# Performance work log

Measured on AMD Instinct MI355X. Metric: run time of the kernel, lower is better.

Reference implementation:

```python
import jax, jax.numpy as jnp
import numpy as np

NUM_SEGMENTS = 4480  # BATCH_SIZE * MAX_ATOMS = 64 * 70
ATOM_DIM = 64
BOND_DIM = 16
N_EDGES = 65536


def setup_inputs() -> dict:
    key = jax.random.key(0)
    k1, k2, k3, k4 = jax.random.split(key, 4)
    atom_feat = jax.random.normal(k1, (NUM_SEGMENTS, ATOM_DIM), dtype=jnp.float32)
    bond_feat = jax.random.normal(k2, (N_EDGES, BOND_DIM), dtype=jnp.float32)
    pair_idx = jax.random.randint(k3, (N_EDGES, 2), 0, NUM_SEGMENTS, dtype=jnp.int64)
    # glorot-uniform style kernel, zero bias (as in add_weight initializers)
    limit = float(np.sqrt(6.0 / (BOND_DIM + ATOM_DIM ** 2)))
    kernel = jax.random.uniform(k4, (BOND_DIM, ATOM_DIM ** 2), dtype=jnp.float32,
                                minval=-limit, maxval=limit)
    bias = jnp.zeros((ATOM_DIM ** 2,), dtype=jnp.float32)
    return {"atom_feat": atom_feat, "bond_feat": bond_feat,
            "pair_idx": pair_idx, "kernel": kernel, "bias": bias}


def reference(atom_feat, bond_feat, pair_idx, kernel, bias):
    atom_dim = atom_feat.shape[-1]
    # dense projection of bond features -> per-edge transform matrices
    bond_transformed = bond_feat @ kernel + bias               # [E, D*D]
    bond_transformed = bond_transformed.reshape(-1, atom_dim, atom_dim)  # [E, D, D]
    # gather neighbor (source) atom features per edge
    neighbor_feat = jnp.take(atom_feat, pair_idx[:, 1].astype(jnp.int32), axis=0)  # [E, D]
    # per-edge matrix-vector product
    messages = jnp.einsum('eij,ej->ei', bond_transformed, neighbor_feat)  # [E, D]
    # scatter-add into destination atoms
    return jax.ops.segment_sum(messages, pair_idx[:, 0].astype(jnp.int32),
                               num_segments=NUM_SEGMENTS)  # [NUM_SEGMENTS, D]
```

## Files before the change

kernel.cpp:

```cpp
#include <hip/hip_runtime.h>

#define NSEG   4480
#define ADIM   64
#define BDIM   16
#define NEDGE  65536
#define DPB    16
#define NBLK   (NSEG / DPB)
#define TPB    1024
#define CAP    64
#define GSP    1096

#define CNT_OFF  (4u << 20)

typedef __bf16 bf16x8 __attribute__((ext_vector_type(8)));
typedef float  f32x4  __attribute__((ext_vector_type(4)));

__device__ __forceinline__ unsigned short f2bf(float f) {
    union { float f; unsigned int i; } c; c.f = f;
    unsigned int x = c.i;
    x += 0x7fffu + ((x >> 16) & 1u);
    return (unsigned short)(x >> 16);
}

union U8 { unsigned short u[8]; bf16x8 v; };

__device__ __forceinline__ bf16x8 pack_bf8(float4 a, float4 b) {
    U8 r;
    r.u[0] = f2bf(a.x); r.u[1] = f2bf(a.y); r.u[2] = f2bf(a.z); r.u[3] = f2bf(a.w);
    r.u[4] = f2bf(b.x); r.u[5] = f2bf(b.y); r.u[6] = f2bf(b.z); r.u[7] = f2bf(b.w);
    return r.v;
}

__global__ __launch_bounds__(256) void scatter_kernel(
    const int* __restrict__ pair, int* __restrict__ cnt, int2* __restrict__ eb)
{
    const int e  = blockIdx.x * 256 + threadIdx.x;
    const int2 p = ((const int2*)pair)[e];
    const int idx = atomicAdd(&cnt[p.x], 1);
    if (idx < CAP) eb[(size_t)p.x * CAP + idx] = make_int2(e, p.y);
}

__global__ __launch_bounds__(TPB) void fused_kernel(
    const float* __restrict__ atom,
    const float* __restrict__ bond,
    const int*   __restrict__ cnt,
    const int2*  __restrict__ eb,
    const float* __restrict__ kern,
    const float* __restrict__ bias,
    float*       __restrict__ out)
{
    __shared__ unsigned short Gs[DPB * GSP];

    const int t    = threadIdx.x;
    const int lane = t & 63;
    const int w    = t >> 6;
    const int dlo  = blockIdx.x * DPB;
    const int d    = dlo + w;

    {
        int n = cnt[d];
        n = n < CAP ? n : CAP;
        const int2 my = eb[(size_t)d * CAP + lane];

        float g[17];
#pragma unroll
        for (int r = 0; r < 17; ++r) g[r] = 0.f;

        int k = 0;
        for (; k + 2 <= n; k += 2) {
            const int e0 = __builtin_amdgcn_readlane(my.x, k);
            const int s0 = __builtin_amdgcn_readlane(my.y, k);
            const int e1 = __builtin_amdgcn_readlane(my.x, k + 1);
            const int s1 = __builtin_amdgcn_readlane(my.y, k + 1);
            const float a0 = atom[(size_t)s0 * ADIM + lane];
            const float a1 = atom[(size_t)s1 * ADIM + lane];
            const float4* b0p = (const float4*)(bond + (size_t)e0 * BDIM);
            const float4* b1p = (const float4*)(bond + (size_t)e1 * BDIM);
            const float4 c0 = b0p[0], c1 = b0p[1], c2 = b0p[2], c3 = b0p[3];
            const float4 d0 = b1p[0], d1 = b1p[1], d2 = b1p[2], d3 = b1p[3];
            const float bb0[16] = { c0.x,c0.y,c0.z,c0.w, c1.x,c1.y,c1.z,c1.w,
                                    c2.x,c2.y,c2.z,c2.w, c3.x,c3.y,c3.z,c3.w };
            const float bb1[16] = { d0.x,d0.y,d0.z,d0.w, d1.x,d1.y,d1.z,d1.w,
                                    d2.x,d2.y,d2.z,d2.w, d3.x,d3.y,d3.z,d3.w };
#pragma unroll
            for (int r = 0; r < 16; ++r) g[r] = fmaf(a0, bb0[r], g[r]);
            g[16] += a0;
#pragma unroll
            for (int r = 0; r < 16; ++r) g[r] = fmaf(a1, bb1[r], g[r]);
            g[16] += a1;
        }
        if (k < n) {
            const int e0 = __builtin_amdgcn_readlane(my.x, k);
            const int s0 = __builtin_amdgcn_readlane(my.y, k);
            const float a0 = atom[(size_t)s0 * ADIM + lane];
            const float4* b0p = (const float4*)(bond + (size_t)e0 * BDIM);
            const float4 c0 = b0p[0], c1 = b0p[1], c2 = b0p[2], c3 = b0p[3];
            const float bb0[16] = { c0.x,c0.y,c0.z,c0.w, c1.x,c1.y,c1.z,c1.w,
                                    c2.x,c2.y,c2.z,c2.w, c3.x,c3.y,c3.z,c3.w };
#pragma unroll
            for (int r = 0; r < 16; ++r) g[r] = fmaf(a0, bb0[r], g[r]);
            g[16] += a0;
        }

#pragma unroll
        for (int r = 0; r < 17; ++r)
            Gs[w * GSP + r * 64 + lane] = f2bf(g[r]);
    }
    __syncthreads();

    if (w < 4) {
        const int m    = lane & 15;
        const int quad = lane >> 4;
        const int c    = w * 16 + m;
        const unsigned short* Ga = Gs + (size_t)m * GSP;

        f32x4 acc = {0.f, 0.f, 0.f, 0.f};

        const float* ks0 = kern + (size_t)c * 64 + quad * 8;
        float4 x0 = *(const float4*)(ks0);
        float4 x1 = *(const float4*)(ks0 + 4);
        float4 y0 = *(const float4*)(ks0 + 32);
        float4 y1 = *(const float4*)(ks0 + 36);

#pragma unroll
        for (int r = 0; r < 17; ++r) {
            float4 nx0, nx1, ny0, ny1;
            if (r + 1 < 17) {
                const float* ns = ((r + 1 < 16) ? (kern + (size_t)(r + 1) * 4096)
                                                : bias)
                                  + (size_t)c * 64 + quad * 8;
                nx0 = *(const float4*)(ns);
                nx1 = *(const float4*)(ns + 4);
                ny0 = *(const float4*)(ns + 32);
                ny1 = *(const float4*)(ns + 36);
            }
            const bf16x8 a0 = *(const bf16x8*)(Ga + r * 64 + quad * 8);
            const bf16x8 a1 = *(const bf16x8*)(Ga + r * 64 + 32 + quad * 8);
            acc = __builtin_amdgcn_mfma_f32_16x16x32_bf16(a0, pack_bf8(x0, x1), acc, 0, 0, 0);
            acc = __builtin_amdgcn_mfma_f32_16x16x32_bf16(a1, pack_bf8(y0, y1), acc, 0, 0, 0);
            x0 = nx0; x1 = nx1; y0 = ny0; y1 = ny1;
        }

#pragma unroll
        for (int rr = 0; rr < 4; ++rr)
            out[(size_t)(dlo + quad * 4 + rr) * ADIM + c] = acc[rr];
    }
}

extern "C" void kernel_launch(void* const* d_in, const int* in_sizes, int n_in,
                              void* d_out, int out_size, void* d_ws, size_t ws_size,
                              hipStream_t stream) {
    const float* atom = (const float*)d_in[0];
    const float* bond = (const float*)d_in[1];
    const int*   pair = (const int*)  d_in[2];
    const float* kern = (const float*)d_in[3];
    const float* bias = (const float*)d_in[4];
    float* out = (float*)d_out;

    int2* eb = (int2*)d_ws;
    int*  cnt = (int*)((char*)d_ws + CNT_OFF);

    hipMemsetAsync(cnt, 0, NSEG * sizeof(int), stream);
    scatter_kernel<<<NEDGE / 256, 256, 0, stream>>>(pair, cnt, eb);
    fused_kernel<<<NBLK, TPB, 0, stream>>>(atom, bond, cnt, eb, kern, bias, out);
}
```

Baseline: 92.19 us.

## Fuse memset, scatter and compute into one cooperative kernel with grid syncs

Result: slower. 240.4 us (+160.8%).

```diff
diff --git a/kernel.cpp b/kernel.cpp
--- a/kernel.cpp
+++ b/kernel.cpp
@@ -1,10 +1,13 @@
 #include <hip/hip_runtime.h>
+#include <hip/hip_cooperative_groups.h>
+
+namespace cg = cooperative_groups;
 
 #define NSEG   4480
 #define ADIM   64
 #define BDIM   16
 #define NEDGE  65536
-#define DPB    16
+#define DPB    32
 #define NBLK   (NSEG / DPB)
 #define TPB    1024
 #define CAP    64
@@ -31,88 +34,118 @@
     return r.v;
 }
 
-__global__ __launch_bounds__(256) void scatter_kernel(
-    const int* __restrict__ pair, int* __restrict__ cnt, int2* __restrict__ eb)
-{
-    const int e  = blockIdx.x * 256 + threadIdx.x;
-    const int2 p = ((const int2*)pair)[e];
-    const int idx = atomicAdd(&cnt[p.x], 1);
-    if (idx < CAP) eb[(size_t)p.x * CAP + idx] = make_int2(e, p.y);
+__device__ __forceinline__ void load_bond16(const float* __restrict__ bond,
+                                            int e, float* bb) {
+    const float4* bp = (const float4*)(bond + (size_t)e * BDIM);
+    const float4 c0 = bp[0], c1 = bp[1], c2 = bp[2], c3 = bp[3];
+    bb[0]=c0.x; bb[1]=c0.y; bb[2]=c0.z; bb[3]=c0.w;
+    bb[4]=c1.x; bb[5]=c1.y; bb[6]=c1.z; bb[7]=c1.w;
+    bb[8]=c2.x; bb[9]=c2.y; bb[10]=c2.z; bb[11]=c2.w;
+    bb[12]=c3.x; bb[13]=c3.y; bb[14]=c3.z; bb[15]=c3.w;
 }
 
 __global__ __launch_bounds__(TPB) void fused_kernel(
     const float* __restrict__ atom,
     const float* __restrict__ bond,
-    const int*   __restrict__ cnt,
-    const int2*  __restrict__ eb,
+    const int*   __restrict__ pair,
     const float* __restrict__ kern,
     const float* __restrict__ bias,
-    float*       __restrict__ out)
+    float*       __restrict__ out,
+    int*         __restrict__ cnt,
+    int2*        __restrict__ eb)
 {
     __shared__ unsigned short Gs[DPB * GSP];
 
+    cg::grid_group grid = cg::this_grid();
+
     const int t    = threadIdx.x;
+    const int gtid = blockIdx.x * TPB + t;
+
+    if (gtid < NSEG) cnt[gtid] = 0;
+    __threadfence();
+    grid.sync();
+
+    if (gtid < NEDGE) {
+        const int2 p = ((const int2*)pair)[gtid];
+        const int idx = atomicAdd(&cnt[p.x], 1);
+        if (idx < CAP) eb[(size_t)p.x * CAP + idx] = make_int2(gtid, p.y);
+    }
+    __threadfence();
+    grid.sync();
+
     const int lane = t & 63;
     const int w    = t >> 6;
     const int dlo  = blockIdx.x * DPB;
-    const int d    = dlo + w;
 
     {
-        int n = cnt[d];
-        n = n < CAP ? n : CAP;
-        const int2 my = eb[(size_t)d * CAP + lane];
-
-        float g[17];
-#pragma unroll
-        for (int r = 0; r < 17; ++r) g[r] = 0.f;
-
-        int k = 0;
-        for (; k + 2 <= n; k += 2) {
-            const int e0 = __builtin_amdgcn_readlane(my.x, k);
-            const int s0 = __builtin_amdgcn_readlane(my.y, k);
-            const int e1 = __builtin_amdgcn_readlane(my.x, k + 1);
-            const int s1 = __builtin_amdgcn_readlane(my.y, k + 1);
-            const float a0 = atom[(size_t)s0 * ADIM + lane];
-            const float a1 = atom[(size_t)s1 * ADIM + lane];
-            const float4* b0p = (const float4*)(bond + (size_t)e0 * BDIM);
-            const float4* b1p = (const float4*)(bond + (size_t)e1 * BDIM);
-            const float4 c0 = b0p[0], c1 = b0p[1], c2 = b0p[2], c3 = b0p[3];
-            const float4 d0 = b1p[0], d1 = b1p[1], d2 = b1p[2], d3 = b1p[3];
-            const float bb0[16] = { c0.x,c0.y,c0.z,c0.w, c1.x,c1.y,c1.z,c1.w,
-                                    c2.x,c2.y,c2.z,c2.w, c3.x,c3.y,c3.z,c3.w };
-            const float bb1[16] = { d0.x,d0.y,d0.z,d0.w, d1.x,d1.y,d1.z,d1.w,
-                                    d2.x,d2.y,d2.z,d2.w, d3.x,d3.y,d3.z,d3.w };
-#pragma unroll
-            for (int r = 0; r < 16; ++r) g[r] = fmaf(a0, bb0[r], g[r]);
-            g[16] += a0;
-#pragma unroll
-            for (int r = 0; r < 16; ++r) g[r] = fmaf(a1, bb1[r], g[r]);
-            g[16] += a1;
+        const int da = dlo + 2 * w;
+        const int db = da + 1;
+        int na = __hip_atomic_load(&cnt[da], __ATOMIC_RELAXED,
+                                   __HIP_MEMORY_SCOPE_AGENT);
+        int nb = __hip_atomic_load(&cnt[db], __ATOMIC_RELAXED,
+                                   __HIP_MEMORY_SCOPE_AGENT);
+        na = na < CAP ? na : CAP;
+        nb = nb < CAP ? nb : CAP;
+        const int2 mya = eb[(size_t)da * CAP + lane];
+        const int2 myb = eb[(size_t)db * CAP + lane];
+
+        float ga[17], gb[17];
+#pragma unroll
+        for (int r = 0; r < 17; ++r) { ga[r] = 0.f; gb[r] = 0.f; }
+
+        const int nmax = na > nb ? na : nb;
+        for (int k = 0; k < nmax; k += 2) {
+            const bool va0 = k < na, va1 = k + 1 < na;
+            const bool vb0 = k < nb, vb1 = k + 1 < nb;
+            int ea0 = __builtin_amdgcn_readlane(mya.x, k);
+            int sa0 = __builtin_amdgcn_readlane(mya.y, k);
+            int ea1 = __builtin_amdgcn_readlane(mya.x, k + 1);
+            int sa1 = __builtin_amdgcn_readlane(mya.y, k + 1);
+            int eb0 = __builtin_amdgcn_readlane(myb.x, k);
+            int sb0 = __builtin_amdgcn_readlane(myb.y, k);
+            int eb1 = __builtin_amdgcn_readlane(myb.x, k + 1);
+            int sb1 = __builtin_amdgcn_readlane(myb.y, k + 1);
+            ea0 = va0 ? ea0 : 0;  sa0 = va0 ? sa0 : 0;
+            ea1 = va1 ? ea1 : 0;  sa1 = va1 ? sa1 : 0;
+            eb0 = vb0 ? eb0 : 0;  sb0 = vb0 ? sb0 : 0;
+            eb1 = vb1 ? eb1 : 0;  sb1 = vb1 ? sb1 : 0;
+
+            const float aa0 = atom[(size_t)sa0 * ADIM + lane] * (va0 ? 1.f : 0.f);
+            const float aa1 = atom[(size_t)sa1 * ADIM + lane] * (va1 ? 1.f : 0.f);
+            const float ab0 = atom[(size_t)sb0 * ADIM + lane] * (vb0 ? 1.f : 0.f);
+            const float ab1 = atom[(size_t)sb1 * ADIM + lane] * (vb1 ? 1.f : 0.f);
+            float ba0[16], ba1[16], bb0[16], bb1[16];
+            load_bond16(bond, ea0, ba0);
+            load_bond16(bond, ea1, ba1);
+            load_bond16(bond, eb0, bb0);
+            load_bond16(bond, eb1, bb1);
+
+#pragma unroll
+            for (int r = 0; r < 16; ++r) {
+                ga[r] = fmaf(aa0, ba0[r], ga[r]);
+                ga[r] = fmaf(aa1, ba1[r], ga[r]);
+                gb[r] = fmaf(ab0, bb0[r], gb[r]);
+                gb[r] = fmaf(ab1, bb1[r], gb[r]);
+            }
+            ga[16] += aa0 + aa1;
+            gb[16] += ab0 + ab1;
         }
-        if (k < n) {
-            const int e0 = __builtin_amdgcn_readlane(my.x, k);
-            const int s0 = __builtin_amdgcn_readlane(my.y, k);
-            const float a0 = atom[(size_t)s0 * ADIM + lane];
-            const float4* b0p = (const float4*)(bond + (size_t)e0 * BDIM);
-            const float4 c0 = b0p[0], c1 = b0p[1], c2 = b0p[2], c3 = b0p[3];
-            const float bb0[16] = { c0.x,c0.y,c0.z,c0.w, c1.x,c1.y,c1.z,c1.w,
-                                    c2.x,c2.y,c2.z,c2.w, c3.x,c3.y,c3.z,c3.w };
-#pragma unroll
-            for (int r = 0; r < 16; ++r) g[r] = fmaf(a0, bb0[r], g[r]);
-            g[16] += a0;
+
+#pragma unroll
+        for (int r = 0; r < 17; ++r) {
+            Gs[(2 * w) * GSP + r * 64 + lane]     = f2bf(ga[r]);
+            Gs[(2 * w + 1) * GSP + r * 64 + lane] = f2bf(gb[r]);
         }
-
-#pragma unroll
-        for (int r = 0; r < 17; ++r)
-            Gs[w * GSP + r * 64 + lane] = f2bf(g[r]);
     }
     __syncthreads();
 
-    if (w < 4) {
+    if (w < 8) {
+        const int mt   = w >> 2;
+        const int ct   = w & 3;
         const int m    = lane & 15;
         const int quad = lane >> 4;
-        const int c    = w * 16 + m;
-        const unsigned short* Ga = Gs + (size_t)m * GSP;
+        const int c    = ct * 16 + m;
+        const unsigned short* Ga = Gs + (size_t)(mt * 16 + m) * GSP;
 
         f32x4 acc = {0.f, 0.f, 0.f, 0.f};
 
@@ -124,7 +157,7 @@
 
 #pragma unroll
         for (int r = 0; r < 17; ++r) {
-            float4 nx0, nx1, ny0, ny1;
+            float4 nx0 = {}, nx1 = {}, ny0 = {}, ny1 = {};
             if (r + 1 < 17) {
                 const float* ns = ((r + 1 < 16) ? (kern + (size_t)(r + 1) * 4096)
                                                 : bias)
@@ -143,7 +176,7 @@
 
 #pragma unroll
         for (int rr = 0; rr < 4; ++rr)
-            out[(size_t)(dlo + quad * 4 + rr) * ADIM + c] = acc[rr];
+            out[(size_t)(dlo + mt * 16 + quad * 4 + rr) * ADIM + c] = acc[rr];
     }
 }
 
@@ -157,10 +190,11 @@
     const float* bias = (const float*)d_in[4];
     float* out = (float*)d_out;
 
-    int2* eb = (int2*)d_ws;
+    int2* eb  = (int2*)d_ws;
     int*  cnt = (int*)((char*)d_ws + CNT_OFF);
 
-    hipMemsetAsync(cnt, 0, NSEG * sizeof(int), stream);
-    scatter_kernel<<<NEDGE / 256, 256, 0, stream>>>(pair, cnt, eb);
-    fused_kernel<<<NBLK, TPB, 0, stream>>>(atom, bond, cnt, eb, kern, bias, out);
-}
+    void* args[] = { (void*)&atom, (void*)&bond, (void*)&pair, (void*)&kern,
+                     (void*)&bias, (void*)&out,  (void*)&cnt,  (void*)&eb };
+    hipLaunchCooperativeKernel(reinterpret_cast<void*>(fused_kernel),
+                               dim3(NBLK), dim3(TPB), args, 0, stream);
+}
```
